# Kernel optimization log

Measured on AMD Instinct MI355X. Metric: run time of the kernel, lower is better.

## Reference

```python
import jax, jax.numpy as jnp
import numpy as np

B, S, D, H, L, V = 2, 1024, 1024, 16, 8, 50257
HD = D // H
FF = 4 * D
EPS = 1e-5


def setup_inputs() -> dict:
    key = jax.random.key(0)
    ks = jax.random.split(key, 16)
    s = 0.02
    return {
        "idx": jax.random.randint(ks[0], (B, S), 0, V, dtype=jnp.int32),
        "tok_emb": jax.random.normal(ks[1], (V, D), jnp.float32) * s,
        "pos_emb": jax.random.normal(ks[2], (S, D), jnp.float32) * s,
        "qkv_w": jax.random.normal(ks[3], (L, 3 * D, D), jnp.float32) * s,
        "proj_w": jax.random.normal(ks[4], (L, D, D), jnp.float32) * s,
        "proj_b": jnp.zeros((L, D), jnp.float32),
        "ln1_s": jnp.ones((L, D), jnp.float32),
        "ln1_b": jnp.zeros((L, D), jnp.float32),
        "fc1_w": jax.random.normal(ks[5], (L, FF, D), jnp.float32) * s,
        "fc1_b": jnp.zeros((L, FF), jnp.float32),
        "fc2_w": jax.random.normal(ks[6], (L, D, FF), jnp.float32) * s,
        "fc2_b": jnp.zeros((L, D), jnp.float32),
        "ln2_s": jnp.ones((L, D), jnp.float32),
        "ln2_b": jnp.zeros((L, D), jnp.float32),
        "lnf_s": jnp.ones((D,), jnp.float32),
        "lnf_b": jnp.zeros((D,), jnp.float32),
        "head_w": jax.random.normal(ks[7], (V, D), jnp.float32) * s,
        "head_b": jnp.zeros((V,), jnp.float32),
    }


def _layer_norm(x, scale, bias):
    mu = jnp.mean(x, axis=-1, keepdims=True)
    var = jnp.mean(jnp.square(x - mu), axis=-1, keepdims=True)
    return (x - mu) * jax.lax.rsqrt(var + EPS) * scale + bias


def _attention(x, qkv_w, proj_w, proj_b, causal):
    b, s, d = x.shape
    qkv = jnp.einsum("bsd,ed->bse", x, qkv_w)            # [B,S,3D]
    qkv = qkv.reshape(b, s, H, 3 * HD)                    # per-head interleaved q,k,v
    q, k, v = jnp.split(qkv, 3, axis=-1)                  # each [B,S,H,HD]
    scale = HD ** -0.5
    scores = jnp.einsum("bqhd,bkhd->bhqk", q, k) * scale  # [B,H,S,S]
    scores = jnp.where(causal, scores, -jnp.inf)
    probs = jax.nn.softmax(scores, axis=-1)
    out = jnp.einsum("bhqk,bkhd->bqhd", probs, v).reshape(b, s, d)
    return out @ proj_w.T + proj_b


def reference(idx, tok_emb, pos_emb, qkv_w, proj_w, proj_b, ln1_s, ln1_b,
              fc1_w, fc1_b, fc2_w, fc2_b, ln2_s, ln2_b, lnf_s, lnf_b,
              head_w, head_b):
    s = idx.shape[1]
    causal = jnp.tril(jnp.ones((s, s), dtype=bool))
    x = tok_emb[idx] + pos_emb[None, :s]                  # [B,S,D]
    for l in range(L):
        h = _layer_norm(x, ln1_s[l], ln1_b[l])
        x = x + _attention(h, qkv_w[l], proj_w[l], proj_b[l], causal)
        h = _layer_norm(x, ln2_s[l], ln2_b[l])
        h = jax.nn.relu(h @ fc1_w[l].T + fc1_b[l]) @ fc2_w[l].T + fc2_b[l]
        x = x + h
    x = _layer_norm(x, lnf_s, lnf_b)
    logits = x @ head_w.T + head_b                        # [B,S,V]
    return logits
```

## Files before the change

### kernel.cpp

```cpp
#include <hip/hip_runtime.h>
#include <hip/hip_bf16.h>
#include <math.h>

#define B_  2
#define S_  1024
#define D_  1024
#define H_  16
#define HD_ 64
#define L_  8
#define FF_ 4096
#define V_  50257
#define M_  (B_ * S_)
#define EPS_ 1e-5f

typedef __attribute__((ext_vector_type(8))) short short8;
typedef __attribute__((ext_vector_type(4))) float f32x4;

__device__ __forceinline__ unsigned short f2bf(float f) {
  union { float f; uint32_t u; } c; c.f = f;
  uint32_t r = (c.u + 0x7FFFu + ((c.u >> 16) & 1u)) >> 16;
  return (unsigned short)r;
}
__device__ __forceinline__ float b2f(unsigned short u) {
  union { uint32_t u; float f; } c; c.u = ((uint32_t)u) << 16;
  return c.f;
}
__device__ __forceinline__ void gll16(const unsigned short* g, unsigned short* lds) {
  __builtin_amdgcn_global_load_lds(
      (const __attribute__((address_space(1))) void*)g,
      (__attribute__((address_space(3))) void*)lds, 16, 0, 0);
}

__global__ __launch_bounds__(256) void embed_kernel(
    const int* __restrict__ idx, const float* __restrict__ tok,
    const float* __restrict__ pos, float* __restrict__ x) {
  int i = blockIdx.x * 256 + threadIdx.x;
  int m = i >> 8;
  int d4 = i & 255;
  int s = m & (S_ - 1);
  int t = idx[m];
  float4 tv = ((const float4*)(tok + (size_t)t * D_))[d4];
  float4 pv = ((const float4*)(pos + (size_t)s * D_))[d4];
  float4 o;
  o.x = tv.x + pv.x; o.y = tv.y + pv.y; o.z = tv.z + pv.z; o.w = tv.w + pv.w;
  ((float4*)(x + (size_t)m * D_))[d4] = o;
}

__global__ __launch_bounds__(256) void cvt_bf16_kernel(
    const float* __restrict__ in, unsigned short* __restrict__ out, int n4) {
  int i = blockIdx.x * 256 + threadIdx.x;
  int stride = gridDim.x * 256;
  for (; i < n4; i += stride) {
    float4 v = ((const float4*)in)[i];
    ushort4 o;
    o.x = f2bf(v.x); o.y = f2bf(v.y); o.z = f2bf(v.z); o.w = f2bf(v.w);
    ((ushort4*)out)[i] = o;
  }
}

__global__ __launch_bounds__(256) void cvt4_kernel(
    const float* __restrict__ s0, const float* __restrict__ s1,
    const float* __restrict__ s2, const float* __restrict__ s3,
    unsigned short* __restrict__ d0, unsigned short* __restrict__ d1,
    unsigned short* __restrict__ d2, unsigned short* __restrict__ d3,
    int n0, int n1, int n2, int n3) {
  int total = n0 + n1 + n2 + n3;
  for (int i = blockIdx.x * 256 + threadIdx.x; i < total; i += gridDim.x * 256) {
    const float* s; unsigned short* d; int j = i;
    if (j < n0)              { s = s0; d = d0; }
    else if ((j -= n0) < n1) { s = s1; d = d1; }
    else if ((j -= n1) < n2) { s = s2; d = d2; }
    else                     { j -= n2; s = s3; d = d3; }
    float4 v = ((const float4*)s)[j];
    ushort4 o;
    o.x = f2bf(v.x); o.y = f2bf(v.y); o.z = f2bf(v.z); o.w = f2bf(v.w);
    ((ushort4*)d)[j] = o;
  }
}

__global__ __launch_bounds__(256) void reduce2_kernel(
    const float* __restrict__ p0, const float* __restrict__ p1,
    const float* __restrict__ bias, float* __restrict__ x, int total4) {
  int i = blockIdx.x * 256 + threadIdx.x;
  if (i >= total4) return;
  float4 a = ((const float4*)p0)[i];
  float4 b = ((const float4*)p1)[i];
  float4 r = ((const float4*)x)[i];
  float4 bb = ((const float4*)bias)[i & 255];
  float4 o;
  o.x = r.x + a.x + b.x + bb.x;
  o.y = r.y + a.y + b.y + bb.y;
  o.z = r.z + a.z + b.z + bb.z;
  o.w = r.w + a.w + b.w + bb.w;
  ((float4*)x)[i] = o;
}

__device__ __forceinline__ float block_sum256(float v, float* red) {
  #pragma unroll
  for (int o = 32; o > 0; o >>= 1) v += __shfl_xor(v, o);
  int w = threadIdx.x >> 6;
  __syncthreads();
  if ((threadIdx.x & 63) == 0) red[w] = v;
  __syncthreads();
  return red[0] + red[1] + red[2] + red[3];
}

__global__ __launch_bounds__(256) void layernorm_kernel(
    const float* __restrict__ x, const float* __restrict__ sc,
    const float* __restrict__ bi, unsigned short* __restrict__ out) {
  __shared__ float red[4];
  int row = blockIdx.x;
  float4 v = ((const float4*)(x + (size_t)row * D_))[threadIdx.x];
  float sum = block_sum256(v.x + v.y + v.z + v.w, red);
  float mu = sum * (1.0f / D_);
  float dx = v.x - mu, dy = v.y - mu, dz = v.z - mu, dw = v.w - mu;
  float sq = block_sum256(dx*dx + dy*dy + dz*dz + dw*dw, red);
  float r = rsqrtf(sq * (1.0f / D_) + EPS_);
  int c = threadIdx.x * 4;
  float4 s4 = *(const float4*)(sc + c);
  float4 b4 = *(const float4*)(bi + c);
  ushort4 o;
  o.x = f2bf(dx * r * s4.x + b4.x);
  o.y = f2bf(dy * r * s4.y + b4.y);
  o.z = f2bf(dz * r * s4.z + b4.z);
  o.w = f2bf(dw * r * s4.w + b4.w);
  ((ushort4*)(out + (size_t)row * D_))[threadIdx.x] = o;
}

#define BM 128
#define BN 128
#define BKg 64

template<bool BIAS, bool RELU, bool OUTBF16>
__global__ __launch_bounds__(256) void gemm_mfma(
    const unsigned short* __restrict__ A, const unsigned short* __restrict__ W,
    const float* __restrict__ bias, void* __restrict__ Cout,
    int M, int N, int K, int lda, int ldc, size_t zstride, int nbx) {
  __shared__ unsigned short As[BM * BKg];
  __shared__ unsigned short Bs[BN * BKg];

  int nwg = gridDim.x;
  int bid = blockIdx.x;
  int q = nwg >> 3, r = nwg & 7;
  int xcd = bid & 7, sub = bid >> 3;
  int swz = (xcd < r ? xcd * (q + 1) : r * (q + 1) + (xcd - r) * q) + sub;
  int by = swz / nbx, bx = swz % nbx;
  int bm = by * BM, bn = bx * BN;

  const size_t Koff = (size_t)blockIdx.y * K;
  const unsigned short* Ab = A + Koff;
  const unsigned short* Wb = W + Koff;

  const int tid = threadIdx.x;
  const int l = tid & 63, w = tid >> 6;
  const int wm = (w >> 1) * 64, wn = (w & 1) * 64;
  const int lr = l >> 3;
  const int lc = (l & 7) << 3;

  const unsigned short* asrc[4];
  const unsigned short* bsrc[4];
  unsigned short* adst[4];
  unsigned short* bdst[4];
  #pragma unroll
  for (int i = 0; i < 4; ++i) {
    int rowa = i * 32 + w * 8;
    asrc[i] = Ab + (size_t)(bm + rowa + lr) * lda + lc;
    adst[i] = As + rowa * BKg;
    int gn = bn + rowa + lr; if (gn >= N) gn = N - 1;
    bsrc[i] = Wb + (size_t)gn * lda + lc;
    bdst[i] = Bs + rowa * BKg;
  }

  f32x4 acc[4][4] = {};
  for (int k0 = 0; k0 < K; k0 += BKg) {
    __syncthreads();
    #pragma unroll
    for (int i = 0; i < 4; ++i) {
      gll16(asrc[i] + k0, adst[i]);
      gll16(bsrc[i] + k0, bdst[i]);
    }
    __syncthreads();
    short8 af[2][4], bfr[2][4];
    #pragma unroll
    for (int ks = 0; ks < 2; ++ks)
      #pragma unroll
      for (int i = 0; i < 4; ++i) {
        af[ks][i]  = *(const short8*)(As + (wm + i * 16 + (l & 15)) * BKg + ks * 32 + (l >> 4) * 8);
        bfr[ks][i] = *(const short8*)(Bs + (wn + i * 16 + (l & 15)) * BKg + ks * 32 + (l >> 4) * 8);
      }
    #pragma unroll
    for (int ks = 0; ks < 2; ++ks)
      #pragma unroll
      for (int i = 0; i < 4; ++i)
        #pragma unroll
        for (int j = 0; j < 4; ++j)
          acc[i][j] = __builtin_amdgcn_mfma_f32_16x16x32_bf16(af[ks][i], bfr[ks][j], acc[i][j], 0, 0, 0);
  }

  const size_t zoff = (size_t)blockIdx.y * zstride;
  const int er = (l >> 4) * 4;
  const int ec = l & 15;
  #pragma unroll
  for (int j = 0; j < 4; ++j) {
    int col = bn + wn + j * 16 + ec;
    if (col < N) {
      float bv = BIAS ? bias[col] : 0.f;
      #pragma unroll
      for (int i = 0; i < 4; ++i) {
        #pragma unroll
        for (int rr = 0; rr < 4; ++rr) {
          int row = bm + wm + i * 16 + er + rr;
          float v = acc[i][j][rr] + bv;
          if (RELU) v = fmaxf(v, 0.f);
          if (OUTBF16) ((unsigned short*)Cout + zoff)[(size_t)row * ldc + col] = f2bf(v);
          else         ((float*)Cout + zoff)[(size_t)row * ldc + col] = v;
        }
      }
    }
  }
}

__global__ __launch_bounds__(256) void attn_mfma_kernel(
    const unsigned short* __restrict__ qkv, unsigned short* __restrict__ out) {
  __shared__ unsigned short Kl[64 * 72];
  __shared__ unsigned short Vt[64 * 72];
  __shared__ unsigned short Pl[4 * 16 * 72];
  const int h = blockIdx.y, b = blockIdx.z;
  const int tile = b ? blockIdx.x : (15 - blockIdx.x);
  const int q0 = tile * 64;
  const int nt = tile + 1;
  const int tid = threadIdx.x;
  const int l = tid & 63, wid = tid >> 6;
  const int g = l >> 4, m15 = l & 15;
  const size_t rs = 3 * D_;
  const unsigned short* base = qkv + (size_t)(b * S_) * rs + h * (3 * HD_);
  const int sk = l;
  const int sd = wid * 16;
  unsigned short* Pw = Pl + wid * 16 * 72;

  const unsigned short* qp = base + (size_t)(q0 + wid * 16 + m15) * rs + g * 8;
  short8 qf0 = *(const short8*)(qp);
  short8 qf1 = *(const short8*)(qp + 32);
  f32x4 acc_o[4] = {};
  float mrun[4] = {-INFINITY, -INFINITY, -INFINITY, -INFINITY};
  float ssum[4] = {0.f, 0.f, 0.f, 0.f};

  const unsigned short* krp = base + (size_t)sk * rs + HD_ + sd;
  short8 kv0 = *(const short8*)(krp);
  short8 kv1 = *(const short8*)(krp + 8);
  short8 vv0 = *(const short8*)(krp + HD_);
  short8 vv1 = *(const short8*)(krp + HD_ + 8);

  for (int kt = 0; kt < nt; ++kt) {
    const int k64 = kt * 64;
    __syncthreads();
    *(short8*)(Kl + sk * 72 + sd) = kv0;
    *(short8*)(Kl + sk * 72 + sd + 8) = kv1;
    #pragma unroll
    for (int e = 0; e < 8; ++e) {
      Vt[(sd + e) * 72 + sk] = (unsigned short)vv0[e];
      Vt[(sd + 8 + e) * 72 + sk] = (unsigned short)vv1[e];
    }
    __syncthreads();
    if (kt + 1 < nt) {
      const unsigned short* krn = base + (size_t)(k64 + 64 + sk) * rs + HD_ + sd;
      kv0 = *(const short8*)(krn);
      kv1 = *(const short8*)(krn + 8);
      vv0 = *(const short8*)(krn + HD_);
      vv1 = *(const short8*)(krn + HD_ + 8);
    }

    f32x4 sc[4] = {};
    #pragma unroll
    for (int j = 0; j < 4; ++j) {
      short8 kf0 = *(const short8*)(Kl + (j * 16 + m15) * 72 + g * 8);
      short8 kf1 = *(const short8*)(Kl + (j * 16 + m15) * 72 + 32 + g * 8);
      sc[j] = __builtin_amdgcn_mfma_f32_16x16x32_bf16(qf0, kf0, sc[j], 0, 0, 0);
      sc[j] = __builtin_amdgcn_mfma_f32_16x16x32_bf16(qf1, kf1, sc[j], 0, 0, 0);
    }

    const bool lastt = (kt == nt - 1);
    #pragma unroll
    for (int rr = 0; rr < 4; ++rr) {
      const int qrow = q0 + wid * 16 + g * 4 + rr;
      float sv[4];
      #pragma unroll
      for (int j = 0; j < 4; ++j) {
        sv[j] = sc[j][rr] * 0.125f;
        if (lastt && (k64 + j * 16 + m15 > qrow)) sv[j] = -1e30f;
      }
      float mx = fmaxf(fmaxf(sv[0], sv[1]), fmaxf(sv[2], sv[3]));
      mx = fmaxf(mx, __shfl_xor(mx, 1));
      mx = fmaxf(mx, __shfl_xor(mx, 2));
      mx = fmaxf(mx, __shfl_xor(mx, 4));
      mx = fmaxf(mx, __shfl_xor(mx, 8));
      float mn = fmaxf(mrun[rr], mx);
      float corr = __expf(mrun[rr] - mn);
      mrun[rr] = mn;
      float ts = 0.f;
      #pragma unroll
      for (int j = 0; j < 4; ++j) {
        float p = __expf(sv[j] - mn);
        ts += p;
        Pw[(g * 4 + rr) * 72 + j * 16 + m15] = f2bf(p);
      }
      ts += __shfl_xor(ts, 1); ts += __shfl_xor(ts, 2);
      ts += __shfl_xor(ts, 4); ts += __shfl_xor(ts, 8);
      ssum[rr] = ssum[rr] * corr + ts;
      #pragma unroll
      for (int j = 0; j < 4; ++j) acc_o[j][rr] *= corr;
    }

    short8 pa0 = *(const short8*)(Pw + m15 * 72 + g * 8);
    short8 pa1 = *(const short8*)(Pw + m15 * 72 + 32 + g * 8);
    #pragma unroll
    for (int j = 0; j < 4; ++j) {
      short8 vb0 = *(const short8*)(Vt + (j * 16 + m15) * 72 + g * 8);
      short8 vb1 = *(const short8*)(Vt + (j * 16 + m15) * 72 + 32 + g * 8);
      acc_o[j] = __builtin_amdgcn_mfma_f32_16x16x32_bf16(pa0, vb0, acc_o[j], 0, 0, 0);
      acc_o[j] = __builtin_amdgcn_mfma_f32_16x16x32_bf16(pa1, vb1, acc_o[j], 0, 0, 0);
    }
  }

  #pragma unroll
  for (int rr = 0; rr < 4; ++rr) {
    const int qrow = q0 + wid * 16 + g * 4 + rr;
    float inv = 1.0f / ssum[rr];
    #pragma unroll
    for (int j = 0; j < 4; ++j)
      out[(size_t)(b * S_ + qrow) * D_ + h * HD_ + j * 16 + m15] =
          f2bf(acc_o[j][rr] * inv);
  }
}

static inline void cvt(const float* src, unsigned short* dst, size_t n, hipStream_t s) {
  int n4 = (int)(n / 4);
  int blocks = (n4 + 255) / 256;
  if (blocks > 2048) blocks = 2048;
  cvt_bf16_kernel<<<blocks, 256, 0, s>>>(src, dst, n4);
}

extern "C" void kernel_launch(void* const* d_in, const int* in_sizes, int n_in,
                              void* d_out, int out_size, void* d_ws, size_t ws_size,
                              hipStream_t stream) {
  const int*   idx    = (const int*)d_in[0];
  const float* tok    = (const float*)d_in[1];
  const float* pos    = (const float*)d_in[2];
  const float* qkv_w  = (const float*)d_in[3];
  const float* proj_w = (const float*)d_in[4];
  const float* proj_b = (const float*)d_in[5];
  const float* ln1_s  = (const float*)d_in[6];
  const float* ln1_b  = (const float*)d_in[7];
  const float* fc1_w  = (const float*)d_in[8];
  const float* fc1_b  = (const float*)d_in[9];
  const float* fc2_w  = (const float*)d_in[10];
  const float* fc2_b  = (const float*)d_in[11];
  const float* ln2_s  = (const float*)d_in[12];
  const float* ln2_b  = (const float*)d_in[13];
  const float* lnf_s  = (const float*)d_in[14];
  const float* lnf_b  = (const float*)d_in[15];
  const float* head_w = (const float*)d_in[16];
  const float* head_b = (const float*)d_in[17];
  float* out = (float*)d_out;

  char* wsb = (char*)d_ws;
  float*          x      = (float*)(wsb);
  unsigned short* h      = (unsigned short*)(wsb + (8u << 20));
  unsigned short* qkvb   = (unsigned short*)(wsb + (12u << 20));
  unsigned short* attnb  = (unsigned short*)(wsb + (24u << 20));
  unsigned short* ff     = (unsigned short*)(wsb + (28u << 20));
  unsigned short* wq     = (unsigned short*)(wsb + (44u << 20));
  unsigned short* wp     = (unsigned short*)(wsb + (50u << 20));
  unsigned short* w1     = (unsigned short*)(wsb + (52u << 20));
  unsigned short* w2     = (unsigned short*)(wsb + (60u << 20));
  float*          part0  = (float*)(wsb + (8u << 20));
  float*          part1  = (float*)(wsb + (16u << 20));

  embed_kernel<<<M_ * D_ / 4 / 256, 256, 0, stream>>>(idx, tok, pos, x);

  const int total4 = M_ * D_ / 4;
  for (int l = 0; l < L_; ++l) {
    layernorm_kernel<<<M_, 256, 0, stream>>>(x, ln1_s + l * D_, ln1_b + l * D_, h);
    cvt4_kernel<<<2048, 256, 0, stream>>>(
        qkv_w + (size_t)l * 3 * D_ * D_, proj_w + (size_t)l * D_ * D_,
        fc1_w + (size_t)l * FF_ * D_, fc2_w + (size_t)l * D_ * FF_,
        wq, wp, w1, w2,
        3 * D_ * D_ / 4, D_ * D_ / 4, FF_ * D_ / 4, D_ * FF_ / 4);
    gemm_mfma<false, false, true><<<dim3(24 * 16, 1), 256, 0, stream>>>(
        h, wq, nullptr, qkvb, M_, 3 * D_, D_, D_, 3 * D_, 0, 24);
    attn_mfma_kernel<<<dim3(16, H_, B_), 256, 0, stream>>>(qkvb, attnb);
    gemm_mfma<false, false, false><<<dim3(8 * 16, 2), 256, 0, stream>>>(
        attnb, wp, nullptr, part0, M_, D_, 512, D_, D_, (size_t)M_ * D_, 8);
    reduce2_kernel<<<2048, 256, 0, stream>>>(part0, part1, proj_b + l * D_, x, total4);
    layernorm_kernel<<<M_, 256, 0, stream>>>(x, ln2_s + l * D_, ln2_b + l * D_, h);
    gemm_mfma<true, true, true><<<dim3(32 * 16, 1), 256, 0, stream>>>(
        h, w1, fc1_b + l * FF_, ff, M_, FF_, D_, D_, FF_, 0, 32);
    gemm_mfma<false, false, false><<<dim3(8 * 16, 2), 256, 0, stream>>>(
        ff, w2, nullptr, part0, M_, D_, 2048, FF_, D_, (size_t)M_ * D_, 8);
    reduce2_kernel<<<2048, 256, 0, stream>>>(part0, part1, fc2_b + l * D_, x, total4);
  }
  layernorm_kernel<<<M_, 256, 0, stream>>>(x, lnf_s, lnf_b, h);

  for (int c0 = 0; c0 < V_; c0 += 8192) {
    int nc = V_ - c0 < 8192 ? V_ - c0 : 8192;
    cvt(head_w + (size_t)c0 * D_, wq, (size_t)nc * D_, stream);
    int nbx = (nc + BN - 1) / BN, nby = M_ / BM;
    gemm_mfma<true, false, false><<<dim3(nbx * nby, 1), 256, 0, stream>>>(
        h, wq, head_b + c0, out + c0, M_, nc, D_, D_, V_, 0, nbx);
  }
}
```

Baseline: 2.028 ms.

## Fuse residual reduce with layernorm, 4-way split-K, 128-key attention tiles

Replaces the separate split-K reduce and layernorm launches with one reduce_ln kernel. It adds bias and four partial sums to the residual, then writes the normalized bf16 activations for the next stage, including the next layer's LN1 and the final LN. The projection and FC2 GEMMs now use 4-way split-K instead of 2-way, which raises grid size at the cost of more partial-sum traffic. The attention kernel processes 128 keys per iteration with larger LDS tiles and raises wave priority around the MFMA sections. The head-weight buffer moves to its own workspace region.

```diff
diff --git a/kernel.cpp b/kernel.cpp
--- a/kernel.cpp
+++ b/kernel.cpp
@@ -20,10 +20,6 @@
   union { float f; uint32_t u; } c; c.f = f;
   uint32_t r = (c.u + 0x7FFFu + ((c.u >> 16) & 1u)) >> 16;
   return (unsigned short)r;
-}
-__device__ __forceinline__ float b2f(unsigned short u) {
-  union { uint32_t u; float f; } c; c.u = ((uint32_t)u) << 16;
-  return c.f;
 }
 __device__ __forceinline__ void gll16(const unsigned short* g, unsigned short* lds) {
   __builtin_amdgcn_global_load_lds(
@@ -76,23 +72,6 @@
     o.x = f2bf(v.x); o.y = f2bf(v.y); o.z = f2bf(v.z); o.w = f2bf(v.w);
     ((ushort4*)d)[j] = o;
   }
-}
-
-__global__ __launch_bounds__(256) void reduce2_kernel(
-    const float* __restrict__ p0, const float* __restrict__ p1,
-    const float* __restrict__ bias, float* __restrict__ x, int total4) {
-  int i = blockIdx.x * 256 + threadIdx.x;
-  if (i >= total4) return;
-  float4 a = ((const float4*)p0)[i];
-  float4 b = ((const float4*)p1)[i];
-  float4 r = ((const float4*)x)[i];
-  float4 bb = ((const float4*)bias)[i & 255];
-  float4 o;
-  o.x = r.x + a.x + b.x + bb.x;
-  o.y = r.y + a.y + b.y + bb.y;
-  o.z = r.z + a.z + b.z + bb.z;
-  o.w = r.w + a.w + b.w + bb.w;
-  ((float4*)x)[i] = o;
 }
 
 __device__ __forceinline__ float block_sum256(float v, float* red) {
@@ -127,6 +106,38 @@
   ((ushort4*)(out + (size_t)row * D_))[threadIdx.x] = o;
 }
 
+__global__ __launch_bounds__(256) void reduce_ln_kernel(
+    const float* __restrict__ parts, const float* __restrict__ bias,
+    float* __restrict__ x, const float* __restrict__ sc,
+    const float* __restrict__ bi, unsigned short* __restrict__ h) {
+  __shared__ float red[4];
+  int row = blockIdx.x;
+  int i = row * 256 + threadIdx.x;
+  float4 v = ((const float4*)x)[i];
+  float4 bb = ((const float4*)bias)[threadIdx.x];
+  v.x += bb.x; v.y += bb.y; v.z += bb.z; v.w += bb.w;
+  #pragma unroll
+  for (int z = 0; z < 4; ++z) {
+    float4 p = ((const float4*)(parts + (size_t)z * M_ * D_))[i];
+    v.x += p.x; v.y += p.y; v.z += p.z; v.w += p.w;
+  }
+  ((float4*)x)[i] = v;
+  float sum = block_sum256(v.x + v.y + v.z + v.w, red);
+  float mu = sum * (1.0f / D_);
+  float dx = v.x - mu, dy = v.y - mu, dz = v.z - mu, dw = v.w - mu;
+  float sq = block_sum256(dx*dx + dy*dy + dz*dz + dw*dw, red);
+  float r = rsqrtf(sq * (1.0f / D_) + EPS_);
+  int c = threadIdx.x * 4;
+  float4 s4 = *(const float4*)(sc + c);
+  float4 b4 = *(const float4*)(bi + c);
+  ushort4 o;
+  o.x = f2bf(dx * r * s4.x + b4.x);
+  o.y = f2bf(dy * r * s4.y + b4.y);
+  o.z = f2bf(dz * r * s4.z + b4.z);
+  o.w = f2bf(dw * r * s4.w + b4.w);
+  ((ushort4*)(h + (size_t)row * D_))[threadIdx.x] = o;
+}
+
 #define BM 128
 #define BN 128
 #define BKg 64
@@ -222,21 +233,20 @@
 
 __global__ __launch_bounds__(256) void attn_mfma_kernel(
     const unsigned short* __restrict__ qkv, unsigned short* __restrict__ out) {
-  __shared__ unsigned short Kl[64 * 72];
-  __shared__ unsigned short Vt[64 * 72];
-  __shared__ unsigned short Pl[4 * 16 * 72];
+  __shared__ unsigned short Kl[128 * 72];
+  __shared__ unsigned short Vt[64 * 136];
+  __shared__ unsigned short Pl[4 * 16 * 136];
   const int h = blockIdx.y, b = blockIdx.z;
   const int tile = b ? blockIdx.x : (15 - blockIdx.x);
   const int q0 = tile * 64;
-  const int nt = tile + 1;
+  const int nt = (q0 + 191) >> 7;
   const int tid = threadIdx.x;
   const int l = tid & 63, wid = tid >> 6;
   const int g = l >> 4, m15 = l & 15;
   const size_t rs = 3 * D_;
   const unsigned short* base = qkv + (size_t)(b * S_) * rs + h * (3 * HD_);
-  const int sk = l;
   const int sd = wid * 16;
-  unsigned short* Pw = Pl + wid * 16 * 72;
+  unsigned short* Pw = Pl + wid * 16 * 136;
 
   const unsigned short* qp = base + (size_t)(q0 + wid * 16 + m15) * rs + g * 8;
   short8 qf0 = *(const short8*)(qp);
@@ -245,51 +255,64 @@
   float mrun[4] = {-INFINITY, -INFINITY, -INFINITY, -INFINITY};
   float ssum[4] = {0.f, 0.f, 0.f, 0.f};
 
-  const unsigned short* krp = base + (size_t)sk * rs + HD_ + sd;
-  short8 kv0 = *(const short8*)(krp);
-  short8 kv1 = *(const short8*)(krp + 8);
-  short8 vv0 = *(const short8*)(krp + HD_);
-  short8 vv1 = *(const short8*)(krp + HD_ + 8);
+  short8 kA0, kA1, kB0, kB1, vA0, vA1, vB0, vB1;
+  {
+    const unsigned short* r0 = base + (size_t)l * rs + HD_ + sd;
+    const unsigned short* r1 = r0 + 64 * rs;
+    kA0 = *(const short8*)(r0);       kA1 = *(const short8*)(r0 + 8);
+    vA0 = *(const short8*)(r0 + HD_); vA1 = *(const short8*)(r0 + HD_ + 8);
+    kB0 = *(const short8*)(r1);       kB1 = *(const short8*)(r1 + 8);
+    vB0 = *(const short8*)(r1 + HD_); vB1 = *(const short8*)(r1 + HD_ + 8);
+  }
 
   for (int kt = 0; kt < nt; ++kt) {
-    const int k64 = kt * 64;
+    const int k128 = kt << 7;
     __syncthreads();
-    *(short8*)(Kl + sk * 72 + sd) = kv0;
-    *(short8*)(Kl + sk * 72 + sd + 8) = kv1;
+    *(short8*)(Kl + l * 72 + sd) = kA0;
+    *(short8*)(Kl + l * 72 + sd + 8) = kA1;
+    *(short8*)(Kl + (64 + l) * 72 + sd) = kB0;
+    *(short8*)(Kl + (64 + l) * 72 + sd + 8) = kB1;
     #pragma unroll
     for (int e = 0; e < 8; ++e) {
-      Vt[(sd + e) * 72 + sk] = (unsigned short)vv0[e];
-      Vt[(sd + 8 + e) * 72 + sk] = (unsigned short)vv1[e];
+      Vt[(sd + e) * 136 + l] = (unsigned short)vA0[e];
+      Vt[(sd + 8 + e) * 136 + l] = (unsigned short)vA1[e];
+      Vt[(sd + e) * 136 + 64 + l] = (unsigned short)vB0[e];
+      Vt[(sd + 8 + e) * 136 + 64 + l] = (unsigned short)vB1[e];
     }
     __syncthreads();
     if (kt + 1 < nt) {
-      const unsigned short* krn = base + (size_t)(k64 + 64 + sk) * rs + HD_ + sd;
-      kv0 = *(const short8*)(krn);
-      kv1 = *(const short8*)(krn + 8);
-      vv0 = *(const short8*)(krn + HD_);
-      vv1 = *(const short8*)(krn + HD_ + 8);
-    }
-
-    f32x4 sc[4] = {};
-    #pragma unroll
-    for (int j = 0; j < 4; ++j) {
+      const unsigned short* r0 = base + (size_t)(k128 + 128 + l) * rs + HD_ + sd;
+      const unsigned short* r1 = r0 + 64 * rs;
+      kA0 = *(const short8*)(r0);       kA1 = *(const short8*)(r0 + 8);
+      vA0 = *(const short8*)(r0 + HD_); vA1 = *(const short8*)(r0 + HD_ + 8);
+      kB0 = *(const short8*)(r1);       kB1 = *(const short8*)(r1 + 8);
+      vB0 = *(const short8*)(r1 + HD_); vB1 = *(const short8*)(r1 + HD_ + 8);
+    }
+
+    f32x4 sc8[8] = {};
+    __builtin_amdgcn_s_setprio(1);
+    #pragma unroll
+    for (int j = 0; j < 8; ++j) {
       short8 kf0 = *(const short8*)(Kl + (j * 16 + m15) * 72 + g * 8);
       short8 kf1 = *(const short8*)(Kl + (j * 16 + m15) * 72 + 32 + g * 8);
-      sc[j] = __builtin_amdgcn_mfma_f32_16x16x32_bf16(qf0, kf0, sc[j], 0, 0, 0);
-      sc[j] = __builtin_amdgcn_mfma_f32_16x16x32_bf16(qf1, kf1, sc[j], 0, 0, 0);
-    }
+      sc8[j] = __builtin_amdgcn_mfma_f32_16x16x32_bf16(qf0, kf0, sc8[j], 0, 0, 0);
+      sc8[j] = __builtin_amdgcn_mfma_f32_16x16x32_bf16(qf1, kf1, sc8[j], 0, 0, 0);
+    }
+    __builtin_amdgcn_s_setprio(0);
 
     const bool lastt = (kt == nt - 1);
     #pragma unroll
     for (int rr = 0; rr < 4; ++rr) {
       const int qrow = q0 + wid * 16 + g * 4 + rr;
-      float sv[4];
-      #pragma unroll
-      for (int j = 0; j < 4; ++j) {
-        sv[j] = sc[j][rr] * 0.125f;
-        if (lastt && (k64 + j * 16 + m15 > qrow)) sv[j] = -1e30f;
+      float sv[8];
+      #pragma unroll
+      for (int j = 0; j < 8; ++j) {
+        sv[j] = sc8[j][rr] * 0.125f;
+        if (lastt && (k128 + j * 16 + m15 > qrow)) sv[j] = -1e30f;
       }
-      float mx = fmaxf(fmaxf(sv[0], sv[1]), fmaxf(sv[2], sv[3]));
+      float mx = sv[0];
+      #pragma unroll
+      for (int j = 1; j < 8; ++j) mx = fmaxf(mx, sv[j]);
       mx = fmaxf(mx, __shfl_xor(mx, 1));
       mx = fmaxf(mx, __shfl_xor(mx, 2));
       mx = fmaxf(mx, __shfl_xor(mx, 4));
@@ -299,10 +322,10 @@
       mrun[rr] = mn;
       float ts = 0.f;
       #pragma unroll
-      for (int j = 0; j < 4; ++j) {
+      for (int j = 0; j < 8; ++j) {
         float p = __expf(sv[j] - mn);
         ts += p;
-        Pw[(g * 4 + rr) * 72 + j * 16 + m15] = f2bf(p);
+        Pw[(g * 4 + rr) * 136 + j * 16 + m15] = f2bf(p);
       }
       ts += __shfl_xor(ts, 1); ts += __shfl_xor(ts, 2);
       ts += __shfl_xor(ts, 4); ts += __shfl_xor(ts, 8);
@@ -311,15 +334,20 @@
       for (int j = 0; j < 4; ++j) acc_o[j][rr] *= corr;
     }
 
-    short8 pa0 = *(const short8*)(Pw + m15 * 72 + g * 8);
-    short8 pa1 = *(const short8*)(Pw + m15 * 72 + 32 + g * 8);
+    short8 pa[4];
+    #pragma unroll
+    for (int ks = 0; ks < 4; ++ks)
+      pa[ks] = *(const short8*)(Pw + m15 * 136 + ks * 32 + g * 8);
+    __builtin_amdgcn_s_setprio(1);
     #pragma unroll
     for (int j = 0; j < 4; ++j) {
-      short8 vb0 = *(const short8*)(Vt + (j * 16 + m15) * 72 + g * 8);
-      short8 vb1 = *(const short8*)(Vt + (j * 16 + m15) * 72 + 32 + g * 8);
-      acc_o[j] = __builtin_amdgcn_mfma_f32_16x16x32_bf16(pa0, vb0, acc_o[j], 0, 0, 0);
-      acc_o[j] = __builtin_amdgcn_mfma_f32_16x16x32_bf16(pa1, vb1, acc_o[j], 0, 0, 0);
-    }
+      #pragma unroll
+      for (int ks = 0; ks < 4; ++ks) {
+        short8 vb = *(const short8*)(Vt + (j * 16 + m15) * 136 + ks * 32 + g * 8);
+        acc_o[j] = __builtin_amdgcn_mfma_f32_16x16x32_bf16(pa[ks], vb, acc_o[j], 0, 0, 0);
+      }
+    }
+    __builtin_amdgcn_s_setprio(0);
   }
 
   #pragma unroll
@@ -373,14 +401,13 @@
   unsigned short* wp     = (unsigned short*)(wsb + (50u << 20));
   unsigned short* w1     = (unsigned short*)(wsb + (52u << 20));
   unsigned short* w2     = (unsigned short*)(wsb + (60u << 20));
-  float*          part0  = (float*)(wsb + (8u << 20));
-  float*          part1  = (float*)(wsb + (16u << 20));
+  float*          parts  = (float*)(wsb + (68u << 20));
+  unsigned short* hw     = (unsigned short*)(wsb + (100u << 20));
 
   embed_kernel<<<M_ * D_ / 4 / 256, 256, 0, stream>>>(idx, tok, pos, x);
-
-  const int total4 = M_ * D_ / 4;
+  layernorm_kernel<<<M_, 256, 0, stream>>>(x, ln1_s, ln1_b, h);
+
   for (int l = 0; l < L_; ++l) {
-    layernorm_kernel<<<M_, 256, 0, stream>>>(x, ln1_s + l * D_, ln1_b + l * D_, h);
     cvt4_kernel<<<2048, 256, 0, stream>>>(
         qkv_w + (size_t)l * 3 * D_ * D_, proj_w + (size_t)l * D_ * D_,
         fc1_w + (size_t)l * FF_ * D_, fc2_w + (size_t)l * D_ * FF_,
@@ -389,23 +416,25 @@
     gemm_mfma<false, false, true><<<dim3(24 * 16, 1), 256, 0, stream>>>(
         h, wq, nullptr, qkvb, M_, 3 * D_, D_, D_, 3 * D_, 0, 24);
     attn_mfma_kernel<<<dim3(16, H_, B_), 256, 0, stream>>>(qkvb, attnb);
-    gemm_mfma<false, false, false><<<dim3(8 * 16, 2), 256, 0, stream>>>(
-        attnb, wp, nullptr, part0, M_, D_, 512, D_, D_, (size_t)M_ * D_, 8);
-    reduce2_kernel<<<2048, 256, 0, stream>>>(part0, part1, proj_b + l * D_, x, total4);
-    layernorm_kernel<<<M_, 256, 0, stream>>>(x, ln2_s + l * D_, ln2_b + l * D_, h);
+    gemm_mfma<false, false, false><<<dim3(8 * 16, 4), 256, 0, stream>>>(
+        attnb, wp, nullptr, parts, M_, D_, 256, D_, D_, (size_t)M_ * D_, 8);
+    reduce_ln_kernel<<<M_, 256, 0, stream>>>(
+        parts, proj_b + l * D_, x, ln2_s + l * D_, ln2_b + l * D_, h);
     gemm_mfma<true, true, true><<<dim3(32 * 16, 1), 256, 0, stream>>>(
         h, w1, fc1_b + l * FF_, ff, M_, FF_, D_, D_, FF_, 0, 32);
-    gemm_mfma<false, false, false><<<dim3(8 * 16, 2), 256, 0, stream>>>(
-        ff, w2, nullptr, part0, M_, D_, 2048, FF_, D_, (size_t)M_ * D_, 8);
-    reduce2_kernel<<<2048, 256, 0, stream>>>(part0, part1, fc2_b + l * D_, x, total4);
-  }
-  layernorm_kernel<<<M_, 256, 0, stream>>>(x, lnf_s, lnf_b, h);
+    gemm_mfma<false, false, false><<<dim3(8 * 16, 4), 256, 0, stream>>>(
+        ff, w2, nullptr, parts, M_, D_, 1024, FF_, D_, (size_t)M_ * D_, 8);
+    const float* ns = (l == L_ - 1) ? lnf_s : ln1_s + (l + 1) * D_;
+    const float* nb = (l == L_ - 1) ? lnf_b : ln1_b + (l + 1) * D_;
+    reduce_ln_kernel<<<M_, 256, 0, stream>>>(
+        parts, fc2_b + l * D_, x, ns, nb, h);
+  }
 
   for (int c0 = 0; c0 < V_; c0 += 8192) {
     int nc = V_ - c0 < 8192 ? V_ - c0 : 8192;
-    cvt(head_w + (size_t)c0 * D_, wq, (size_t)nc * D_, stream);
+    cvt(head_w + (size_t)c0 * D_, hw, (size_t)nc * D_, stream);
     int nbx = (nc + BN - 1) / BN, nby = M_ / BM;
     gemm_mfma<true, false, false><<<dim3(nbx * nby, 1), 256, 0, stream>>>(
-        h, wq, head_b + c0, out + c0, M_, nc, D_, D_, V_, 0, nbx);
-  }
-}
+        h, hw, head_b + c0, out + c0, M_, nc, D_, D_, V_, 0, nbx);
+  }
+}
```

After: 1.884 ms. -7.1%, faster.
